# Kernel optimization log

Measured on AMD Instinct MI355X. Metric: run time of the kernel, lower is better.

The kernel has to match this reference:

```python
import jax, jax.numpy as jnp
import numpy as np

NE = 14  # NUM_ELEMENTS
CH = 18  # NE + density, gravity, fluid_momentum, cloner_assign
EMPTY, WALL, SAND, WATER, GAS, WOOD, ICE, FIRE, PLANT, STONE, LAVA, ACID, DUST, CLONER = range(14)
DENSITY = np.array([0., 5., 3., 2., -1., 5., 5., 0., 5., 4., 3., 2., 3., 5.], np.float32)
GRAVITY = np.array([1., 0., 1., 1., 1., 0., 1., 1., 0., 1., 1., 1., 1., 0.], np.float32)

# direction vectors for the 2-channel velocity field, layout [vy, vx]
UP = jnp.array([-1., 0.], jnp.float32).reshape(1, 2, 1, 1)
DOWN = jnp.array([1., 0.], jnp.float32).reshape(1, 2, 1, 1)
LEFT = jnp.array([0., -1.], jnp.float32).reshape(1, 2, 1, 1)
RIGHT = jnp.array([0., 1.], jnp.float32).reshape(1, 2, 1, 1)

get_above = lambda x: jnp.roll(x, 1, axis=2)
get_below = lambda x: jnp.roll(x, -1, axis=2)
get_left = lambda x: jnp.roll(x, 1, axis=3)
get_right = lambda x: jnp.roll(x, -1, axis=3)

def conv3x3(x):
    k = jnp.ones((1, 1, 3, 3), x.dtype)
    return jax.lax.conv_general_dilated(x, k, (1, 1), 'SAME',
        dimension_numbers=('NCHW', 'OIHW', 'NCHW'))

def get_bool(world, e):
    return world[:, e:e+1] == 1

def get_elem(world, e):
    return world[:, e:e+1]

def behavior_acid(world, rand_interact, elem_table):
    acid_rand = rand_interact < 0.2
    is_block = ~(get_bool(world, EMPTY) | get_bool(world, WALL) | get_bool(world, ACID) | get_bool(world, CLONER))
    is_acid = get_bool(world, ACID)
    does_acid = (is_acid & acid_rand & get_below(is_block)) | (is_acid & acid_rand & get_above(is_block))
    does_block = (is_block & get_above(acid_rand) & get_above(is_acid)) | (is_block & get_below(acid_rand) & get_below(is_acid))
    dd = does_acid | does_block
    empty_vec = elem_table[EMPTY].reshape(1, CH, 1, 1)
    return jnp.where(dd, empty_vec, world)

def behavior_fire(world, rand_interact, rand_element, velocity_field, elem_table):
    burn = rand_interact
    fire_and_lava = get_elem(world, FIRE) + get_elem(world, LAVA)
    has_fire_nb = conv3x3(fire_and_lava) > 0
    db_wood = get_bool(world, WOOD) & (burn < 0.05)
    db_plant = get_bool(world, PLANT) & (burn < 0.2)
    db_gas = get_bool(world, GAS) & (burn < 0.2)
    db_dust = get_bool(world, DUST)
    db_ice = get_bool(world, ICE) & (burn < 0.2) & has_fire_nb
    does_burn = (db_wood | db_plant | db_gas | db_dust) & has_fire_nb
    bfn = (does_burn & has_fire_nb).astype(world.dtype)
    dfn = (db_dust & has_fire_nb).astype(world.dtype)
    velocity_field = velocity_field - 2. * get_left(bfn) * LEFT - 2. * get_above(bfn) * UP \
        - 2. * get_below(bfn) * DOWN - 2. * get_right(bfn) * RIGHT \
        - 20. * get_left(dfn) * LEFT - 20. * get_above(dfn) * UP \
        - 20. * get_below(dfn) * DOWN - 20. * get_right(dfn) * RIGHT
    fire_vec = elem_table[FIRE].reshape(1, CH, 1, 1)
    water_vec = elem_table[WATER].reshape(1, CH, 1, 1)
    empty_vec = elem_table[EMPTY].reshape(1, CH, 1, 1)
    world = jnp.where(does_burn, fire_vec, world)
    world = jnp.where(db_ice, water_vec, world)
    burnables = get_elem(world, WOOD) + get_elem(world, PLANT) + get_elem(world, GAS) + get_elem(world, DUST)
    fire_with_burnable_nb = conv3x3(burnables) * fire_and_lava
    in_fire_range = conv3x3(fire_with_burnable_nb + get_elem(world, LAVA))
    db_empty = get_bool(world, EMPTY) & (in_fire_range > 0) & (burn < 0.3)
    world = jnp.where(db_empty, fire_vec, world)
    has_burnable_nb = conv3x3(burnables)
    fire_empty = get_bool(world, FIRE) & (rand_element < 0.4) & (has_burnable_nb == 0)
    world = jnp.where(fire_empty, empty_vec, world)
    return world, velocity_field

def behavior_fluid_flow(world, rand_movement, did_gravity):
    new_mom = jnp.zeros_like(world[:, :1])
    not_dg = did_gravity <= 0
    for elem in (EMPTY, WATER, GAS, LAVA, ACID):
        for fall_left in (True, False):
            fluid_mom = world[:, NE+2:NE+3]
            fall_dir = (rand_movement + fluid_mom + new_mom) > 0.5
            gdir = get_left if fall_left else get_right
            gnot = get_right if fall_left else get_left
            is_el = world[:, elem:elem+1] == 1
            is_r_el = gnot(is_el)
            density = world[:, NE:NE+1]
            is_match = fall_dir if fall_left else ~fall_dir
            is_r_match = gnot(is_match)
            l_dens_lo = (density - gdir(density)) > 0
            r_dens_hi = (gnot(density) - density) > 0
            is_grav = world[:, NE+1:NE+2] == 1
            l_grav = gdir(is_grav) & is_grav
            r_grav = gnot(is_grav) & is_grav
            dbl = is_match & is_el & not_dg & l_dens_lo & l_grav
            dbr = is_r_match & is_r_el & gnot(not_dg) & r_dens_hi & r_grav
            new_mom = new_mom + dbr * (2.0 if fall_left else -2.0)
            wl, wr = gdir(world), gnot(world)
            # interp2: (~a & ~b)*world + a*wl + b*wr (sums if both fire)
            world = (~(dbl | dbr)) * world + dbl * wl + dbr * wr
    return world.at[:, NE+2:NE+3].set(new_mom)

def behavior_cloner(world, elem_table):
    is_not_cloner = ~get_bool(world, CLONER)
    labels = jnp.argmax(world[:, :NE], axis=1)[:, None].astype(world.dtype)
    for gdir in (get_below, get_above, get_left, get_right):
        ca = world[:, NE+3:NE+4]
        is_cl_empty = get_bool(world, CLONER) & ((ca == 0) | (ca == 13))
        new_ca = (~(is_cl_empty | is_not_cloner)) * ca + is_cl_empty * gdir(labels)
        world = world.at[:, NE+3:NE+4].set(new_ca)
    ca = world[:, NE+3:NE+4]
    vec = elem_table[world[:, NE+3].astype(jnp.int32)]          # [B,H,W,CH]
    vec = jnp.transpose(vec, (0, 3, 1, 2))                       # [B,CH,H,W]
    is_cl_assigned = get_bool(world, CLONER) & ((ca != 0) & (ca != 13))
    for gdir in (get_below, get_above, get_left, get_right):
        is_dir = gdir(is_cl_assigned) & get_bool(world, EMPTY)
        world = jnp.where(is_dir, gdir(vec), world)
    return world

def make_elem_table():
    t = np.zeros((NE, CH), np.float32)
    t[np.arange(NE), np.arange(NE)] = 1.
    t[:, NE] = DENSITY
    t[:, NE+1] = GRAVITY
    return jnp.asarray(t)

def setup_inputs():
    key = jax.random.key(0)
    ks = jax.random.split(key, 5)
    B, H, W = 4, 512, 512
    elem_table = make_elem_table()
    ids = jax.random.randint(ks[0], (B, H, W), 0, NE)
    world = jnp.transpose(elem_table[ids], (0, 3, 1, 2))  # [B,CH,H,W]
    return {
        'world': world,
        'rand_movement': jax.random.uniform(ks[1], (B, 1, H, W), jnp.float32),
        'rand_interact': jax.random.uniform(ks[2], (B, 1, H, W), jnp.float32),
        'rand_element': jax.random.uniform(ks[3], (B, 1, H, W), jnp.float32),
        'velocity_field': jax.random.normal(ks[4], (B, 2, H, W), jnp.float32),
        'did_gravity': jnp.zeros((B, 1, H, W), jnp.float32),
        'elem_table': elem_table,
    }

def reference(world, rand_movement, rand_interact, rand_element, velocity_field, did_gravity, elem_table):
    world = behavior_acid(world, rand_interact, elem_table)
    world, velocity_field = behavior_fire(world, rand_interact, rand_element, velocity_field, elem_table)
    world = behavior_fluid_flow(world, rand_movement, did_gravity)
    world = behavior_cloner(world, elem_table)
    return world, velocity_field
```

## Files before the change

### kernel.cpp

```cpp
#include <hip/hip_runtime.h>

#define E_EMPTY  0
#define E_WALL   1
#define E_SAND   2
#define E_WATER  3
#define E_GAS    4
#define E_WOOD   5
#define E_ICE    6
#define E_FIRE   7
#define E_PLANT  8
#define E_STONE  9
#define E_LAVA   10
#define E_ACID   11
#define E_DUST   12
#define E_CLONER 13

#define CH 18
#define HW (512*512)
#define NPIX (4*HW)
#define NWORLD (4*CH*HW)

typedef unsigned long long u64;
#define ONE8 0x0101010101010101ULL
#define K7F  0x7F7F7F7F7F7F7F7FULL
#define H80  0x8080808080808080ULL
#define LOWN 0x0F0F0F0F0F0F0F0FULL

__constant__ float c_dens[14] = {0.f,5.f,3.f,2.f,-1.f,5.f,5.f,0.f,5.f,4.f,3.f,2.f,3.f,5.f};
__constant__ float c_grav[14] = {1.f,0.f,1.f,1.f,1.f,0.f,1.f,1.f,0.f,1.f,1.f,1.f,1.f,0.f};

__device__ __forceinline__ u64 bcast(int k) { return ONE8 * (unsigned)k; }
__device__ __forceinline__ u64 eqb(u64 x, int k) {
  u64 y = x ^ bcast(k);
  return ((~(y + K7F)) >> 7) & ONE8;
}
__device__ __forceinline__ u64 geb(u64 a, u64 b) { return (((a | H80) - b) >> 7) & ONE8; }
__device__ __forceinline__ u64 gtb(u64 a, u64 b) { return ONE8 ^ geb(b, a); }
__device__ __forceinline__ u64 mexp(u64 m) { return (m << 8) - m; }
__device__ __forceinline__ u64 fl01w(u64 e) { return eqb(e, E_FIRE) | eqb(e, E_LAVA); }
__device__ __forceinline__ u64 burn01w(u64 b) {
  u64 e = b & LOWN;
  return eqb(e,E_WOOD) | eqb(e,E_PLANT) | eqb(e,E_GAS) | eqb(e,E_DUST);
}
__device__ __forceinline__ u64 isblkw(u64 e) {
  return ONE8 ^ (eqb(e,E_EMPTY) | eqb(e,E_WALL) | eqb(e,E_ACID) | eqb(e,E_CLONER));
}

__device__ __forceinline__ unsigned char decode1(float d, float g, float f, float wa,
                                                 float wo, float pl, float sa, float lv, float wt) {
  if (g < 0.5f) {
    if (wa > 0.5f) return E_WALL;
    if (wo > 0.5f) return E_WOOD;
    if (pl > 0.5f) return E_PLANT;
    return E_CLONER;
  }
  int di = (int)d;
  if (di == 0) return (f > 0.5f) ? E_FIRE : E_EMPTY;
  if (di == 5) return E_ICE;
  if (di == 4) return E_STONE;
  if (di < 0)  return E_GAS;
  if (di == 3) { if (sa > 0.5f) return E_SAND; if (lv > 0.5f) return E_LAVA; return E_DUST; }
  return (wt > 0.5f) ? E_WATER : E_ACID;
}

__global__ __launch_bounds__(256) void k_prep(const float* __restrict__ w,
                                              const float* __restrict__ ri,
                                              const float* __restrict__ re,
                                              const float* __restrict__ rm,
                                              const float* __restrict__ dg,
                                              unsigned char* __restrict__ e0,
                                              unsigned char* __restrict__ rb) {
  int g = blockIdx.x * 256 + threadIdx.x;
  int base = g << 2;
  int b = base >> 18;
  int r = base & (HW - 1);
  const float* wb = w + (size_t)b * CH * HW + r;
  float4 D  = *reinterpret_cast<const float4*>(wb + (size_t)14 * HW);
  float4 G  = *reinterpret_cast<const float4*>(wb + (size_t)15 * HW);
  float4 F  = *reinterpret_cast<const float4*>(wb + (size_t)7  * HW);
  float4 WA = *reinterpret_cast<const float4*>(wb + (size_t)1  * HW);
  float4 WO = *reinterpret_cast<const float4*>(wb + (size_t)5  * HW);
  float4 PL = *reinterpret_cast<const float4*>(wb + (size_t)8  * HW);
  float4 SA = *reinterpret_cast<const float4*>(wb + (size_t)2  * HW);
  float4 LV = *reinterpret_cast<const float4*>(wb + (size_t)10 * HW);
  float4 WT = *reinterpret_cast<const float4*>(wb + (size_t)3  * HW);
  uchar4 e;
  e.x = decode1(D.x, G.x, F.x, WA.x, WO.x, PL.x, SA.x, LV.x, WT.x);
  e.y = decode1(D.y, G.y, F.y, WA.y, WO.y, PL.y, SA.y, LV.y, WT.y);
  e.z = decode1(D.z, G.z, F.z, WA.z, WO.z, PL.z, SA.z, LV.z, WT.z);
  e.w = decode1(D.w, G.w, F.w, WA.w, WO.w, PL.w, SA.w, LV.w, WT.w);
  *reinterpret_cast<uchar4*>(e0 + base) = e;

  float4 RI = *reinterpret_cast<const float4*>(ri + base);
  float4 RE = *reinterpret_cast<const float4*>(re + base);
  float4 RM = *reinterpret_cast<const float4*>(rm + base);
  float4 DG = *reinterpret_cast<const float4*>(dg + base);
  uchar4 q;
  q.x = (RI.x<0.05f?1:0)|(RI.x<0.2f?2:0)|(RI.x<0.3f?4:0)|(RE.x<0.4f?8:0)|(RM.x>0.5f?16:0)|(DG.x<=0.f?32:0);
  q.y = (RI.y<0.05f?1:0)|(RI.y<0.2f?2:0)|(RI.y<0.3f?4:0)|(RE.y<0.4f?8:0)|(RM.y>0.5f?16:0)|(DG.y<=0.f?32:0);
  q.z = (RI.z<0.05f?1:0)|(RI.z<0.2f?2:0)|(RI.z<0.3f?4:0)|(RE.z<0.4f?8:0)|(RM.z>0.5f?16:0)|(DG.z<=0.f?32:0);
  q.w = (RI.w<0.05f?1:0)|(RI.w<0.2f?2:0)|(RI.w<0.3f?4:0)|(RE.w<0.4f?8:0)|(RM.w>0.5f?16:0)|(DG.w<=0.f?32:0);
  *reinterpret_cast<uchar4*>(rb + base) = q;
}

__device__ __forceinline__ void fstep(bool left, int el, u64& E, u64& D, u64& Gv, u64& mom,
                                      u64 rmB, u64 ndB, u64 ndW, u64 ndE,
                                      int laneL, int laneR) {
  u64 fd = geb(mom, bcast(33)) | (eqb(mom, 32) & rmB);
  int pkT = (int)(E >> 56) | (((int)(D >> 56)) << 8) | (((int)(Gv >> 56)) << 11)
          | (((int)(fd >> 56)) << 12);
  int pkB = ((int)E & 255) | (((int)D & 255) << 8) | (((int)Gv & 1) << 11)
          | (((int)fd & 1) << 12);
  int pL = __shfl(pkT, laneL, 64);
  int pR = __shfl(pkB, laneR, 64);
  u64 EW = (E << 8) | (u64)(pL & 255);
  u64 DW = (D << 8) | (u64)((pL >> 8) & 7);
  u64 GW = (Gv << 8) | (u64)((pL >> 11) & 1);
  u64 EE = (E >> 8) | ((u64)(pR & 255) << 56);
  u64 DE = (D >> 8) | ((u64)((pR >> 8) & 7) << 56);
  u64 GE = (Gv >> 8) | ((u64)((pR >> 11) & 1) << 56);
  u64 dbl, dbr;
  if (left) {
    u64 fdE = (fd >> 8) | ((u64)((pR >> 12) & 1) << 56);
    dbl = fd  & eqb(E, el)  & ndB & gtb(D, DW) & GW & Gv;
    dbr = fdE & eqb(EE, el) & ndE & gtb(DE, D) & GE & Gv;
    mom += dbr << 1;
    u64 Ml = mexp(dbl), Mr = mexp(dbr), kp = ~(Ml | Mr);
    E  = (EW & Ml) | (EE & Mr) | (E  & kp);
    D  = (DW & Ml) | (DE & Mr) | (D  & kp);
    Gv = (GW & Ml) | (GE & Mr) | (Gv & kp);
  } else {
    u64 fdW = (fd << 8) | (u64)((pL >> 12) & 1);
    dbl = (fd  ^ ONE8) & eqb(E, el)  & ndB & gtb(D, DE) & GE & Gv;
    dbr = (fdW ^ ONE8) & eqb(EW, el) & ndW & gtb(DW, D) & GW & Gv;
    mom -= dbr << 1;
    u64 Ml = mexp(dbl), Mr = mexp(dbr), kp = ~(Ml | Mr);
    E  = (EE & Ml) | (EW & Mr) | (E  & kp);
    D  = (DE & Ml) | (DW & Mr) | (D  & kp);
    Gv = (GE & Ml) | (GW & Mr) | (Gv & kp);
  }
}

__global__ __launch_bounds__(512) void k_rest(const unsigned char* __restrict__ e0g,
                                              const unsigned char* __restrict__ rbg,
                                              const float* __restrict__ vin,
                                              float* __restrict__ out) {
  __shared__ u64 RBs[14][64];
  __shared__ u64 As[14][64];
  __shared__ u64 EASs[12][64];
  __shared__ u64 B1s[10][64];
  __shared__ u64 HBNs[8][64];
  __shared__ u64 EFs[6][64];
  __shared__ u64 ELs[6][64];
  __shared__ u64 nmsW[2][64];

  int tid = threadIdx.x;
  int blk = blockIdx.x;
  int b = blk >> 8;
  int ty = (blk & 255) << 1;
  int bbase = b * HW;
  float* vout = out + NWORLD;

  if (tid < 448) {
    int l = tid >> 5, ch = (tid & 31) << 4;
    int gy = (ty + l - 6) & 511;
    int gi = bbase + (gy << 9) + ch;
    *reinterpret_cast<uint4*>(reinterpret_cast<char*>(&As[l][0]) + ch) =
        *reinterpret_cast<const uint4*>(e0g + gi);
    *reinterpret_cast<uint4*>(reinterpret_cast<char*>(&RBs[l][0]) + ch) =
        *reinterpret_cast<const uint4*>(rbg + gi);
  }
  __syncthreads();

  int w = tid & 63, rsl = tid >> 6;

  #pragma unroll
  for (int l = rsl; l < 12; l += 8) {
    u64 eu = As[l][w], ec = As[l+1][w], ed = As[l+2][w];
    u64 ru = RBs[l][w], rc = RBs[l+1][w], rd = RBs[l+2][w];
    u64 ibu = isblkw(eu), ibc = isblkw(ec), ibd = isblkw(ed);
    u64 da = eqb(ec,E_ACID) & ((rc>>1)&ONE8) & (ibd | ibu);
    u64 db = ibc & ((((ru>>1)&ONE8) & eqb(eu,E_ACID)) | (((rd>>1)&ONE8) & eqb(ed,E_ACID)));
    EASs[l][w] = ec & ~mexp(da | db);
  }
  __syncthreads();

  #pragma unroll
  for (int l = rsl; l < 12; l += 8) {
    u64 C = fl01w(EASs[l][w]);
    u64 Lf = w ? fl01w(EASs[l][w-1]) : 0;
    u64 Rf = (w < 63) ? fl01w(EASs[l][w+1]) : 0;
    As[l][w] = C | (C<<8) | (Lf>>56) | (C>>8) | (Rf<<56);
  }
  __syncthreads();

  #pragma unroll
  for (int l = rsl; l < 10; l += 8) {
    int a = (ty + l - 4) & 511;
    u64 hf = As[l+1][w];
    if (a != 0)   hf |= As[l][w];
    if (a != 511) hf |= As[l+2][w];
    u64 e = EASs[l+1][w], rb = RBs[l+2][w];
    u64 m0 = rb & ONE8, m1 = (rb>>1) & ONE8;
    u64 eqd = eqb(e,E_DUST);
    u64 dbv = (eqb(e,E_WOOD)&m0) | (eqb(e,E_PLANT)&m1) | (eqb(e,E_GAS)&m1) | eqd;
    u64 burn = dbv & hf;
    u64 ice = eqb(e,E_ICE) & m1 & hf;
    u64 Mb = mexp(burn), Mi = mexp(ice) & ~Mb;
    u64 e1 = (bcast(E_FIRE) & Mb) | (bcast(E_WATER) & Mi) | (e & ~(Mb|Mi));
    B1s[l][w] = e1 | (burn<<4) | ((eqd & hf)<<5);
  }
  __syncthreads();

  #pragma unroll
  for (int l = rsl; l < 10; l += 8) {
    u64 C = burn01w(B1s[l][w]);
    u64 Lb = w ? burn01w(B1s[l][w-1]) : 0;
    u64 Rb = (w < 63) ? burn01w(B1s[l][w+1]) : 0;
    As[l][w] = C + ((C<<8)|(Lb>>56)) + ((C>>8)|(Rb<<56));
  }
  __syncthreads();

  {
    int l = rsl;
    int a = (ty + l - 3) & 511;
    u64 s = As[l+1][w];
    if (a != 0)   s += As[l][w];
    if (a != 511) s += As[l+2][w];
    HBNs[l][w] = s;
  }
  __syncthreads();

  {
    int l = rsl;
    As[l][w] = (HBNs[l][w] & mexp(fl01w(EASs[l+2][w]))) + eqb(B1s[l+1][w] & LOWN, E_LAVA);
  }
  __syncthreads();

  {
    int l = rsl;
    u64 C = As[l][w];
    u64 Lg = w ? As[l][w-1] : 0;
    u64 Rg = (w < 63) ? As[l][w+1] : 0;
    EASs[l][w] = C + ((C<<8)|(Lg>>56)) + ((C>>8)|(Rg<<56));
  }
  __syncthreads();

  if (rsl < 6) {
    int l = rsl;
    int a = (ty + l - 2) & 511;
    u64 ifr = EASs[l+1][w];
    if (a != 0)   ifr += EASs[l][w];
    if (a != 511) ifr += EASs[l+2][w];
    u64 nz = ((ifr + K7F) >> 7) & ONE8;
    u64 e1 = B1s[l+2][w] & LOWN;
    u64 rb = RBs[l+4][w];
    u64 dbe = eqb(e1,E_EMPTY) & nz & ((rb>>2)&ONE8);
    u64 e2 = e1 | (bcast(E_FIRE) & mexp(dbe));
    u64 fe = eqb(e2,E_FIRE) & ((rb>>3)&ONE8) & eqb(HBNs[l+1][w], 0);
    EFs[l][w] = e2 & ~mexp(fe);
  }
  {
    const unsigned char* B1b = reinterpret_cast<const unsigned char*>(&B1s[0][0]);
    int x = tid;
    int xl1 = (x + 511) & 511, xr1 = (x + 1) & 511;
    #pragma unroll
    for (int r = 0; r < 2; ++r) {
      int gy = ty + r;
      int fu  = B1b[(r+3)*512 + x];
      int fd_ = B1b[(r+5)*512 + x];
      int flf = B1b[(r+4)*512 + xl1];
      int frt = B1b[(r+4)*512 + xr1];
      float vy = vin[(size_t)(b*2+0)*HW + (gy<<9) + x];
      vy = vy + 2.0f*(float)((fu>>4)&1);   vy = vy - 2.0f*(float)((fd_>>4)&1);
      vy = vy + 20.0f*(float)((fu>>5)&1);  vy = vy - 20.0f*(float)((fd_>>5)&1);
      float vx = vin[(size_t)(b*2+1)*HW + (gy<<9) + x];
      vx = vx + 2.0f*(float)((flf>>4)&1);  vx = vx - 2.0f*(float)((frt>>4)&1);
      vx = vx + 20.0f*(float)((flf>>5)&1); vx = vx - 20.0f*(float)((frt>>5)&1);
      vout[(size_t)(b*2+0)*HW + (gy<<9) + x] = vy;
      vout[(size_t)(b*2+1)*HW + (gy<<9) + x] = vx;
    }
  }
  __syncthreads();

  {
    int w8 = tid >> 6, lane = tid & 63;
    if (w8 < 6) {
      u64 E = EFs[w8][lane];
      u64 rbW = RBs[w8 + 4][lane];
      u64 rmB = (rbW >> 4) & ONE8;
      u64 ndB = (rbW >> 5) & ONE8;
      u64 g1 = eqb(E,1), g5 = eqb(E,5), g6 = eqb(E,6), g8 = eqb(E,8), g13 = eqb(E,13);
      u64 m5 = g1|g5|g6|g8|g13;
      u64 m3 = eqb(E,2)|eqb(E,10)|eqb(E,12);
      u64 m2 = eqb(E,3)|eqb(E,11);
      u64 D = ONE8 + ((m5<<2)+m5) + ((m3<<1)+m3) + (m2<<1) + (eqb(E,9)<<2) - eqb(E,4);
      u64 Gv = ONE8 ^ (g1|g5|g8|g13);
      u64 mom = bcast(32);

      int laneL = (lane + 63) & 63, laneR = (lane + 1) & 63;
      int ndpk = (int)(ndB >> 56) | (((int)ndB & 1) << 1);
      u64 ndTopL = (u64)(__shfl(ndpk, laneL, 64) & 1);
      u64 ndBotR = (u64)((__shfl(ndpk, laneR, 64) >> 1) & 1);
      u64 ndW = (ndB << 8) | ndTopL;
      u64 ndE = (ndB >> 8) | (ndBotR << 56);

      #pragma unroll
      for (int ei = 0; ei < 5; ++ei) {
        const int el = (ei==0) ? E_EMPTY : (ei==1) ? E_WATER : (ei==2) ? E_GAS
                     : (ei==3) ? E_LAVA  : E_ACID;
        fstep(true,  el, E, D, Gv, mom, rmB, ndB, ndW, ndE, laneL, laneR);
        fstep(false, el, E, D, Gv, mom, rmB, ndB, ndW, ndE, laneL, laneR);
      }
      ELs[w8][lane] = E;
      if (w8 == 2 || w8 == 3) nmsW[w8 - 2][lane] = mom;
    }
  }
  __syncthreads();

  {
    const unsigned char* ELb = reinterpret_cast<const unsigned char*>(&ELs[0][0]);
    const unsigned char* NMb = reinterpret_cast<const unsigned char*>(&nmsW[0][0]);
    int q = tid & 255, h = tid >> 8;
    int r = q >> 7;
    int x0 = (q & 127) << 2;
    const int DY[4] = {1, -1, 0, 0};
    const int DX[4] = {0, 0, -1, 1};
    int eo[4]; float mom[4], cao[4];
    #pragma unroll
    for (int k = 0; k < 4; ++k) {
      int xx = x0 + k;
      int ry = r + 2;
      int ec = ELb[ry*512 + xx];
      float m = (float)((int)NMb[r*512 + xx] - 32);
      int e = ec; float ca = 0.f;
      if (ec == E_CLONER) {
        int c = ELb[(ry+1)*512 + xx];
        if (c==0||c==13) c = ELb[(ry-1)*512 + xx];
        if (c==0||c==13) c = ELb[ry*512 + ((xx+511)&511)];
        if (c==0||c==13) c = ELb[ry*512 + ((xx+1)&511)];
        ca = (float)c;
      } else if (ec == E_EMPTY) {
        #pragma unroll
        for (int d = 0; d < 4; ++d) {
          int qy = ry + DY[d], qx = (xx + DX[d]) & 511;
          if (ELb[qy*512 + qx] == E_CLONER) {
            int c = ELb[(qy+1)*512 + qx];
            if (c==0||c==13) c = ELb[(qy-1)*512 + qx];
            if (c==0||c==13) c = ELb[qy*512 + ((qx+511)&511)];
            if (c==0||c==13) c = ELb[qy*512 + ((qx+1)&511)];
            if (c != 0 && c != 13) { e = c; m = 0.f; break; }
          }
        }
      }
      eo[k] = e; mom[k] = m; cao[k] = ca;
    }
    float* ob = out + (size_t)b * CH * HW + ((ty + r) << 9) + x0;
    int c0 = h * 9, c1 = c0 + 9;
    for (int c = c0; c < c1; ++c) {
      float4 v;
      if (c < 14) {
        v = make_float4(eo[0]==c ? 1.f : 0.f, eo[1]==c ? 1.f : 0.f,
                        eo[2]==c ? 1.f : 0.f, eo[3]==c ? 1.f : 0.f);
      } else if (c == 14) {
        v = make_float4(c_dens[eo[0]], c_dens[eo[1]], c_dens[eo[2]], c_dens[eo[3]]);
      } else if (c == 15) {
        v = make_float4(c_grav[eo[0]], c_grav[eo[1]], c_grav[eo[2]], c_grav[eo[3]]);
      } else if (c == 16) {
        v = make_float4(mom[0], mom[1], mom[2], mom[3]);
      } else {
        v = make_float4(cao[0], cao[1], cao[2], cao[3]);
      }
      *reinterpret_cast<float4*>(ob + (size_t)c * HW) = v;
    }
  }
}

extern "C" void kernel_launch(void* const* d_in, const int* in_sizes, int n_in,
                              void* d_out, int out_size, void* d_ws, size_t ws_size,
                              hipStream_t stream) {
  const float* world = (const float*)d_in[0];
  const float* rm    = (const float*)d_in[1];
  const float* ri    = (const float*)d_in[2];
  const float* re    = (const float*)d_in[3];
  const float* vel   = (const float*)d_in[4];
  const float* dg    = (const float*)d_in[5];
  float* out = (float*)d_out;

  char* ws = (char*)d_ws;
  unsigned char* e0 = (unsigned char*)ws;
  unsigned char* rb = e0 + NPIX;

  hipLaunchKernelGGL(k_prep, dim3(NPIX/1024), dim3(256), 0, stream,
                     world, ri, re, rm, dg, e0, rb);
  hipLaunchKernelGGL(k_rest, dim3(4*256), dim3(512), 0, stream,
                     e0, rb, vel, out);
}
```

Before: 52.09 us.

## Process four rows per block and fuse horizontal/vertical stencil passes

```diff
diff --git a/kernel.cpp b/kernel.cpp
--- a/kernel.cpp
+++ b/kernel.cpp
@@ -145,27 +145,27 @@
                                               const unsigned char* __restrict__ rbg,
                                               const float* __restrict__ vin,
                                               float* __restrict__ out) {
-  __shared__ u64 RBs[14][64];
-  __shared__ u64 As[14][64];
-  __shared__ u64 EASs[12][64];
-  __shared__ u64 B1s[10][64];
-  __shared__ u64 HBNs[8][64];
-  __shared__ u64 EFs[6][64];
-  __shared__ u64 ELs[6][64];
-  __shared__ u64 nmsW[2][64];
+  __shared__ u64 E0s[16][64];
+  __shared__ u64 RBs[16][64];
+  __shared__ u64 EASs[14][64];
+  __shared__ u64 B1s[12][64];
+  __shared__ u64 HBNs[10][64];
+  __shared__ u64 EFs[8][64];
+  __shared__ u64 ELs[8][64];
+  __shared__ u64 nmsW[4][64];
 
   int tid = threadIdx.x;
   int blk = blockIdx.x;
-  int b = blk >> 8;
-  int ty = (blk & 255) << 1;
+  int b = blk >> 7;
+  int ty = (blk & 127) << 2;
   int bbase = b * HW;
   float* vout = out + NWORLD;
 
-  if (tid < 448) {
+  {
     int l = tid >> 5, ch = (tid & 31) << 4;
     int gy = (ty + l - 6) & 511;
     int gi = bbase + (gy << 9) + ch;
-    *reinterpret_cast<uint4*>(reinterpret_cast<char*>(&As[l][0]) + ch) =
+    *reinterpret_cast<uint4*>(reinterpret_cast<char*>(&E0s[l][0]) + ch) =
         *reinterpret_cast<const uint4*>(e0g + gi);
     *reinterpret_cast<uint4*>(reinterpret_cast<char*>(&RBs[l][0]) + ch) =
         *reinterpret_cast<const uint4*>(rbg + gi);
@@ -175,8 +175,8 @@
   int w = tid & 63, rsl = tid >> 6;
 
   #pragma unroll
-  for (int l = rsl; l < 12; l += 8) {
-    u64 eu = As[l][w], ec = As[l+1][w], ed = As[l+2][w];
+  for (int l = rsl; l < 14; l += 8) {
+    u64 eu = E0s[l][w], ec = E0s[l+1][w], ed = E0s[l+2][w];
     u64 ru = RBs[l][w], rc = RBs[l+1][w], rd = RBs[l+2][w];
     u64 ibu = isblkw(eu), ibc = isblkw(ec), ibd = isblkw(ed);
     u64 da = eqb(ec,E_ACID) & ((rc>>1)&ONE8) & (ibd | ibu);
@@ -187,19 +187,23 @@
 
   #pragma unroll
   for (int l = rsl; l < 12; l += 8) {
-    u64 C = fl01w(EASs[l][w]);
-    u64 Lf = w ? fl01w(EASs[l][w-1]) : 0;
-    u64 Rf = (w < 63) ? fl01w(EASs[l][w+1]) : 0;
-    As[l][w] = C | (C<<8) | (Lf>>56) | (C>>8) | (Rf<<56);
-  }
-  __syncthreads();
-
-  #pragma unroll
-  for (int l = rsl; l < 10; l += 8) {
     int a = (ty + l - 4) & 511;
-    u64 hf = As[l+1][w];
-    if (a != 0)   hf |= As[l][w];
-    if (a != 511) hf |= As[l+2][w];
+    u64 C1 = fl01w(EASs[l+1][w]);
+    u64 L1 = w ? fl01w(EASs[l+1][w-1]) : 0;
+    u64 R1 = (w < 63) ? fl01w(EASs[l+1][w+1]) : 0;
+    u64 hf = C1 | (C1<<8) | (L1>>56) | (C1>>8) | (R1<<56);
+    if (a != 0) {
+      u64 C0 = fl01w(EASs[l][w]);
+      u64 L0 = w ? fl01w(EASs[l][w-1]) : 0;
+      u64 R0 = (w < 63) ? fl01w(EASs[l][w+1]) : 0;
+      hf |= C0 | (C0<<8) | (L0>>56) | (C0>>8) | (R0<<56);
+    }
+    if (a != 511) {
+      u64 C2 = fl01w(EASs[l+2][w]);
+      u64 L2 = w ? fl01w(EASs[l+2][w-1]) : 0;
+      u64 R2 = (w < 63) ? fl01w(EASs[l+2][w+1]) : 0;
+      hf |= C2 | (C2<<8) | (L2>>56) | (C2>>8) | (R2<<56);
+    }
     u64 e = EASs[l+1][w], rb = RBs[l+2][w];
     u64 m0 = rb & ONE8, m1 = (rb>>1) & ONE8;
     u64 eqd = eqb(e,E_DUST);
@@ -214,44 +218,48 @@
 
   #pragma unroll
   for (int l = rsl; l < 10; l += 8) {
-    u64 C = burn01w(B1s[l][w]);
-    u64 Lb = w ? burn01w(B1s[l][w-1]) : 0;
-    u64 Rb = (w < 63) ? burn01w(B1s[l][w+1]) : 0;
-    As[l][w] = C + ((C<<8)|(Lb>>56)) + ((C>>8)|(Rb<<56));
+    int a = (ty + l - 3) & 511;
+    u64 C1 = burn01w(B1s[l+1][w]);
+    u64 L1 = w ? burn01w(B1s[l+1][w-1]) : 0;
+    u64 R1 = (w < 63) ? burn01w(B1s[l+1][w+1]) : 0;
+    u64 s = C1 + ((C1<<8)|(L1>>56)) + ((C1>>8)|(R1<<56));
+    if (a != 0) {
+      u64 C0 = burn01w(B1s[l][w]);
+      u64 L0 = w ? burn01w(B1s[l][w-1]) : 0;
+      u64 R0 = (w < 63) ? burn01w(B1s[l][w+1]) : 0;
+      s += C0 + ((C0<<8)|(L0>>56)) + ((C0>>8)|(R0<<56));
+    }
+    if (a != 511) {
+      u64 C2 = burn01w(B1s[l+2][w]);
+      u64 L2 = w ? burn01w(B1s[l+2][w-1]) : 0;
+      u64 R2 = (w < 63) ? burn01w(B1s[l+2][w+1]) : 0;
+      s += C2 + ((C2<<8)|(L2>>56)) + ((C2>>8)|(R2<<56));
+    }
+    HBNs[l][w] = s;
   }
   __syncthreads();
 
   {
     int l = rsl;
-    int a = (ty + l - 3) & 511;
-    u64 s = As[l+1][w];
-    if (a != 0)   s += As[l][w];
-    if (a != 511) s += As[l+2][w];
-    HBNs[l][w] = s;
-  }
-  __syncthreads();
-
-  {
-    int l = rsl;
-    As[l][w] = (HBNs[l][w] & mexp(fl01w(EASs[l+2][w]))) + eqb(B1s[l+1][w] & LOWN, E_LAVA);
-  }
-  __syncthreads();
-
-  {
-    int l = rsl;
-    u64 C = As[l][w];
-    u64 Lg = w ? As[l][w-1] : 0;
-    u64 Rg = (w < 63) ? As[l][w+1] : 0;
-    EASs[l][w] = C + ((C<<8)|(Lg>>56)) + ((C>>8)|(Rg<<56));
-  }
-  __syncthreads();
-
-  if (rsl < 6) {
-    int l = rsl;
     int a = (ty + l - 2) & 511;
-    u64 ifr = EASs[l+1][w];
-    if (a != 0)   ifr += EASs[l][w];
-    if (a != 511) ifr += EASs[l+2][w];
+    #define GW_(g, ww) ((HBNs[g][ww] & mexp(fl01w(EASs[(g)+2][ww]))) + eqb(B1s[(g)+1][ww] & LOWN, E_LAVA))
+    u64 C1 = GW_(l+1, w);
+    u64 L1 = w ? GW_(l+1, w-1) : 0;
+    u64 R1 = (w < 63) ? GW_(l+1, w+1) : 0;
+    u64 ifr = C1 + ((C1<<8)|(L1>>56)) + ((C1>>8)|(R1<<56));
+    if (a != 0) {
+      u64 C0 = GW_(l, w);
+      u64 L0 = w ? GW_(l, w-1) : 0;
+      u64 R0 = (w < 63) ? GW_(l, w+1) : 0;
+      ifr += C0 + ((C0<<8)|(L0>>56)) + ((C0>>8)|(R0<<56));
+    }
+    if (a != 511) {
+      u64 C2 = GW_(l+2, w);
+      u64 L2 = w ? GW_(l+2, w-1) : 0;
+      u64 R2 = (w < 63) ? GW_(l+2, w+1) : 0;
+      ifr += C2 + ((C2<<8)|(L2>>56)) + ((C2>>8)|(R2<<56));
+    }
+    #undef GW_
     u64 nz = ((ifr + K7F) >> 7) & ONE8;
     u64 e1 = B1s[l+2][w] & LOWN;
     u64 rb = RBs[l+4][w];
@@ -265,7 +273,7 @@
     int x = tid;
     int xl1 = (x + 511) & 511, xr1 = (x + 1) & 511;
     #pragma unroll
-    for (int r = 0; r < 2; ++r) {
+    for (int r = 0; r < 4; ++r) {
       int gy = ty + r;
       int fu  = B1b[(r+3)*512 + x];
       int fd_ = B1b[(r+5)*512 + x];
@@ -285,45 +293,42 @@
 
   {
     int w8 = tid >> 6, lane = tid & 63;
-    if (w8 < 6) {
-      u64 E = EFs[w8][lane];
-      u64 rbW = RBs[w8 + 4][lane];
-      u64 rmB = (rbW >> 4) & ONE8;
-      u64 ndB = (rbW >> 5) & ONE8;
-      u64 g1 = eqb(E,1), g5 = eqb(E,5), g6 = eqb(E,6), g8 = eqb(E,8), g13 = eqb(E,13);
-      u64 m5 = g1|g5|g6|g8|g13;
-      u64 m3 = eqb(E,2)|eqb(E,10)|eqb(E,12);
-      u64 m2 = eqb(E,3)|eqb(E,11);
-      u64 D = ONE8 + ((m5<<2)+m5) + ((m3<<1)+m3) + (m2<<1) + (eqb(E,9)<<2) - eqb(E,4);
-      u64 Gv = ONE8 ^ (g1|g5|g8|g13);
-      u64 mom = bcast(32);
-
-      int laneL = (lane + 63) & 63, laneR = (lane + 1) & 63;
-      int ndpk = (int)(ndB >> 56) | (((int)ndB & 1) << 1);
-      u64 ndTopL = (u64)(__shfl(ndpk, laneL, 64) & 1);
-      u64 ndBotR = (u64)((__shfl(ndpk, laneR, 64) >> 1) & 1);
-      u64 ndW = (ndB << 8) | ndTopL;
-      u64 ndE = (ndB >> 8) | (ndBotR << 56);
-
-      #pragma unroll
-      for (int ei = 0; ei < 5; ++ei) {
-        const int el = (ei==0) ? E_EMPTY : (ei==1) ? E_WATER : (ei==2) ? E_GAS
-                     : (ei==3) ? E_LAVA  : E_ACID;
-        fstep(true,  el, E, D, Gv, mom, rmB, ndB, ndW, ndE, laneL, laneR);
-        fstep(false, el, E, D, Gv, mom, rmB, ndB, ndW, ndE, laneL, laneR);
-      }
-      ELs[w8][lane] = E;
-      if (w8 == 2 || w8 == 3) nmsW[w8 - 2][lane] = mom;
-    }
+    u64 E = EFs[w8][lane];
+    u64 rbW = RBs[w8 + 4][lane];
+    u64 rmB = (rbW >> 4) & ONE8;
+    u64 ndB = (rbW >> 5) & ONE8;
+    u64 g1 = eqb(E,1), g5 = eqb(E,5), g8 = eqb(E,8), g13 = eqb(E,13);
+    u64 m5 = g1|g5|eqb(E,6)|g8|g13;
+    u64 m3 = eqb(E,2)|eqb(E,10)|eqb(E,12);
+    u64 m2 = eqb(E,3)|eqb(E,11);
+    u64 D = ONE8 + ((m5<<2)+m5) + ((m3<<1)+m3) + (m2<<1) + (eqb(E,9)<<2) - eqb(E,4);
+    u64 Gv = ONE8 ^ (g1|g5|g8|g13);
+    u64 mom = bcast(32);
+
+    int laneL = (lane + 63) & 63, laneR = (lane + 1) & 63;
+    int ndpk = (int)(ndB >> 56) | (((int)ndB & 1) << 1);
+    u64 ndTopL = (u64)(__shfl(ndpk, laneL, 64) & 1);
+    u64 ndBotR = (u64)((__shfl(ndpk, laneR, 64) >> 1) & 1);
+    u64 ndW = (ndB << 8) | ndTopL;
+    u64 ndE = (ndB >> 8) | (ndBotR << 56);
+
+    #pragma unroll
+    for (int ei = 0; ei < 5; ++ei) {
+      const int el = (ei==0) ? E_EMPTY : (ei==1) ? E_WATER : (ei==2) ? E_GAS
+                   : (ei==3) ? E_LAVA  : E_ACID;
+      fstep(true,  el, E, D, Gv, mom, rmB, ndB, ndW, ndE, laneL, laneR);
+      fstep(false, el, E, D, Gv, mom, rmB, ndB, ndW, ndE, laneL, laneR);
+    }
+    ELs[w8][lane] = E;
+    if (w8 >= 2 && w8 < 6) nmsW[w8 - 2][lane] = mom;
   }
   __syncthreads();
 
   {
     const unsigned char* ELb = reinterpret_cast<const unsigned char*>(&ELs[0][0]);
     const unsigned char* NMb = reinterpret_cast<const unsigned char*>(&nmsW[0][0]);
-    int q = tid & 255, h = tid >> 8;
-    int r = q >> 7;
-    int x0 = (q & 127) << 2;
+    int r = tid >> 7;
+    int x0 = (tid & 127) << 2;
     const int DY[4] = {1, -1, 0, 0};
     const int DX[4] = {0, 0, -1, 1};
     int eo[4]; float mom[4], cao[4];
@@ -356,23 +361,20 @@
       eo[k] = e; mom[k] = m; cao[k] = ca;
     }
     float* ob = out + (size_t)b * CH * HW + ((ty + r) << 9) + x0;
-    int c0 = h * 9, c1 = c0 + 9;
-    for (int c = c0; c < c1; ++c) {
-      float4 v;
-      if (c < 14) {
-        v = make_float4(eo[0]==c ? 1.f : 0.f, eo[1]==c ? 1.f : 0.f,
-                        eo[2]==c ? 1.f : 0.f, eo[3]==c ? 1.f : 0.f);
-      } else if (c == 14) {
-        v = make_float4(c_dens[eo[0]], c_dens[eo[1]], c_dens[eo[2]], c_dens[eo[3]]);
-      } else if (c == 15) {
-        v = make_float4(c_grav[eo[0]], c_grav[eo[1]], c_grav[eo[2]], c_grav[eo[3]]);
-      } else if (c == 16) {
-        v = make_float4(mom[0], mom[1], mom[2], mom[3]);
-      } else {
-        v = make_float4(cao[0], cao[1], cao[2], cao[3]);
-      }
+    #pragma unroll
+    for (int c = 0; c < 14; ++c) {
+      float4 v = make_float4(eo[0]==c ? 1.f : 0.f, eo[1]==c ? 1.f : 0.f,
+                             eo[2]==c ? 1.f : 0.f, eo[3]==c ? 1.f : 0.f);
       *reinterpret_cast<float4*>(ob + (size_t)c * HW) = v;
     }
+    *reinterpret_cast<float4*>(ob + (size_t)14*HW) =
+        make_float4(c_dens[eo[0]], c_dens[eo[1]], c_dens[eo[2]], c_dens[eo[3]]);
+    *reinterpret_cast<float4*>(ob + (size_t)15*HW) =
+        make_float4(c_grav[eo[0]], c_grav[eo[1]], c_grav[eo[2]], c_grav[eo[3]]);
+    *reinterpret_cast<float4*>(ob + (size_t)16*HW) =
+        make_float4(mom[0], mom[1], mom[2], mom[3]);
+    *reinterpret_cast<float4*>(ob + (size_t)17*HW) =
+        make_float4(cao[0], cao[1], cao[2], cao[3]);
   }
 }
 
@@ -393,6 +395,6 @@
 
   hipLaunchKernelGGL(k_prep, dim3(NPIX/1024), dim3(256), 0, stream,
                      world, ri, re, rm, dg, e0, rb);
-  hipLaunchKernelGGL(k_rest, dim3(4*256), dim3(512), 0, stream,
+  hipLaunchKernelGGL(k_rest, dim3(4*128), dim3(512), 0, stream,
                      e0, rb, vel, out);
 }
```

Measured after the change: 44.48 us. -14.6%, faster.
